# Kernel optimization log

Hardware: AMD Instinct MI355X
Metric: run time of the kernel (lower is better)

Reference implementation:

```python
import jax, jax.numpy as jnp
import numpy as np

NUM_HEADS = 16
D_MODEL = 1024
D_K = D_MODEL // NUM_HEADS
B, S = 2, 2048


def setup_inputs() -> dict:
    key = jax.random.key(0)
    ks = jax.random.split(key, 10)
    q = jax.random.normal(ks[0], (B, S, D_MODEL), dtype=jnp.float32)
    k = jax.random.normal(ks[1], (B, S, D_MODEL), dtype=jnp.float32)
    v = jax.random.normal(ks[2], (B, S, D_MODEL), dtype=jnp.float32)
    # causal mask, 1 = keep, 0 = masked (masked_fill(mask==0, -1e9))
    mask = jnp.tril(jnp.ones((S, S), dtype=jnp.int32))[None, None, :, :]
    # Linear weights ~ N(0, 0.02); biases left at torch default-ish small uniform
    std = 0.02
    Wq = jax.random.normal(ks[3], (D_MODEL, D_MODEL), dtype=jnp.float32) * std
    Wk = jax.random.normal(ks[4], (D_MODEL, D_MODEL), dtype=jnp.float32) * std
    Wv = jax.random.normal(ks[5], (D_MODEL, D_MODEL), dtype=jnp.float32) * std
    bound = 1.0 / np.sqrt(D_MODEL)
    bq = jax.random.uniform(ks[6], (D_MODEL,), jnp.float32, -bound, bound)
    bk = jax.random.uniform(ks[7], (D_MODEL,), jnp.float32, -bound, bound)
    bv = jax.random.uniform(ks[8], (D_MODEL,), jnp.float32, -bound, bound)
    return {"q": q, "k": k, "v": v, "mask": mask,
            "Wq": Wq, "bq": bq, "Wk": Wk, "bk": bk, "Wv": Wv, "bv": bv}


def reference(q, k, v, mask, Wq, bq, Wk, bk, Wv, bv):
    # projections (torch Linear: x @ W.T + b), split heads -> [B, H, S, Dk]
    def proj(x, W, b):
        y = x @ W.T + b
        return y.reshape(B, S, NUM_HEADS, D_K).transpose(0, 2, 1, 3)

    qh, kh, vh = proj(q, Wq, bq), proj(k, Wk, bk), proj(v, Wv, bv)
    scores = jnp.einsum('bhqd,bhkd->bhqk', qh, kh) / jnp.sqrt(jnp.float32(D_K))
    scores = jnp.where(mask == 0, jnp.float32(-1e9), scores)
    p = jax.nn.softmax(scores, axis=-1)
    # dropout is identity in eval mode
    x = jnp.einsum('bhqk,bhkd->bhqd', p, vh)  # [B, H, S, Dk]
    return x.transpose(0, 2, 1, 3).reshape(B, S, D_MODEL)
```

## Files before the change

### kernel.cpp

```cpp
#include <hip/hip_runtime.h>

#define B_ 2
#define H_ 16
#define S_ 2048
#define DM 1024
#define DK 64
#define NX (4096 * 1024)
#define NW (1024 * 1024)

typedef unsigned short u16;
typedef __attribute__((ext_vector_type(8))) short bf16x8;
typedef __attribute__((ext_vector_type(8))) unsigned short u16x8;
typedef __attribute__((ext_vector_type(4))) unsigned short u16x4;
typedef __attribute__((ext_vector_type(2))) unsigned int u32x2;
typedef __attribute__((ext_vector_type(4))) unsigned int u32x4;
typedef __attribute__((ext_vector_type(4))) float f32x4;
typedef __attribute__((ext_vector_type(16))) float f32x16;

__device__ inline u16 f2bf(float f) {
  union { float f; unsigned int u; } c; c.f = f;
  unsigned int u = c.u;
  u += 0x7fffu + ((u >> 16) & 1u);
  return (u16)(u >> 16);
}

__device__ inline u16x8 cvt8(const float* __restrict__ src) {
  const float4 a = *reinterpret_cast<const float4*>(src);
  const float4 b = *reinterpret_cast<const float4*>(src + 4);
  u16x8 r;
  r[0] = f2bf(a.x); r[1] = f2bf(a.y); r[2] = f2bf(a.z); r[3] = f2bf(a.w);
  r[4] = f2bf(b.x); r[5] = f2bf(b.y); r[6] = f2bf(b.z); r[7] = f2bf(b.w);
  return r;
}

__device__ inline void glds16(const u16* g, u16* l) {
  __builtin_amdgcn_global_load_lds(
      (const __attribute__((address_space(1))) unsigned int*)g,
      (__attribute__((address_space(3))) unsigned int*)l, 16, 0, 0);
}

__device__ inline unsigned cvtpk(float lo, float hi) {
  unsigned r;
  asm("v_cvt_pk_bf16_f32 %0, %1, %2" : "=v"(r) : "v"(lo), "v"(hi));
  return r;
}

#if __has_builtin(__builtin_amdgcn_permlane32_swap)
__device__ inline void plswap(unsigned& a, unsigned& b) {
  auto r = __builtin_amdgcn_permlane32_swap(a, b, false, false);
  a = r[0]; b = r[1];
}
#else
__device__ inline void plswap(unsigned& a, unsigned& b) {
  const unsigned pa = (unsigned)__shfl_xor((int)a, 32, 64);
  const unsigned pb = (unsigned)__shfl_xor((int)b, 32, 64);
  const bool hi = (threadIdx.x & 32) != 0;
  const unsigned na = hi ? pb : a;
  const unsigned nb = hi ? b : pa;
  a = na; b = nb;
}
#endif

__global__ __launch_bounds__(256) void cvt_kernel(
    const float* __restrict__ q, const float* __restrict__ k, const float* __restrict__ v,
    const float* __restrict__ Wq, const float* __restrict__ Wk, const float* __restrict__ Wv,
    u16* __restrict__ Xq, u16* __restrict__ Xk, u16* __restrict__ Xv,
    u16* __restrict__ Wqb, u16* __restrict__ Wkb, u16* __restrict__ Wvb)
{
  const int t = blockIdx.y;
  const float* src = (t == 0) ? q : (t == 1) ? k : (t == 2) ? v
                   : (t == 3) ? Wq : (t == 4) ? Wk : Wv;
  u16* dst = (t == 0) ? Xq : (t == 1) ? Xk : (t == 2) ? Xv
           : (t == 3) ? Wqb : (t == 4) ? Wkb : Wvb;
  const int n = (t < 3) ? NX : NW;
  const int idx = (blockIdx.x * 256 + threadIdx.x) * 8;
  if (idx >= n) return;
  *reinterpret_cast<u16x8*>(&dst[idx]) = cvt8(&src[idx]);
}

__global__ __launch_bounds__(256) void proj_kernel(
    const u16* __restrict__ Xq, const u16* __restrict__ Xk, const u16* __restrict__ Xv,
    const u16* __restrict__ Wqb, const u16* __restrict__ Wkb, const u16* __restrict__ Wvb,
    const float* __restrict__ bq, const float* __restrict__ bk, const float* __restrict__ bv,
    u16* __restrict__ Qh, u16* __restrict__ Kh, u16* __restrict__ Vh)
{
  const int z = blockIdx.z;
  const u16* X      = (z == 0) ? Xq : (z == 1) ? Xk : Xv;
  const u16* W      = (z == 0) ? Wqb : (z == 1) ? Wkb : Wvb;
  const float* bias = (z == 0) ? bq : (z == 1) ? bk : bv;
  u16* out          = (z == 0) ? Qh : (z == 1) ? Kh : Vh;
  const float scale = (z == 0) ? 0.18033688f : 1.0f;

  __shared__ __align__(16) u16 Xs[128 * 32];
  __shared__ __align__(16) u16 Ws[128 * 32];

  const int tid = threadIdx.x;
  const int lane = tid & 63;
  const int w = tid >> 6;
  const int wy = w >> 1, wx = w & 1;
  const int m0 = blockIdx.y * 128;
  const int n0 = blockIdx.x * 128;
  const int ml = lane & 15;
  const int qd = lane >> 4;

  f32x4 acc[4][4] = {};

  for (int kb = 0; kb < DM; kb += 32) {
    __syncthreads();
    #pragma unroll
    for (int p = 0; p < 2; ++p) {
      const int c = p * 4 + w;
      const int row = c * 16 + (lane >> 2);
      const int col = kb + (lane & 3) * 8;
      glds16(&X[(size_t)(m0 + row) * DM + col], &Xs[c * 512]);
      glds16(&W[(size_t)(n0 + row) * DM + col], &Ws[c * 512]);
    }
    __syncthreads();
    bf16x8 a[4], bfr[4];
    #pragma unroll
    for (int i = 0; i < 4; ++i)
      a[i] = *reinterpret_cast<const bf16x8*>(&Xs[(wy * 64 + i * 16 + ml) * 32 + qd * 8]);
    #pragma unroll
    for (int j = 0; j < 4; ++j)
      bfr[j] = *reinterpret_cast<const bf16x8*>(&Ws[(wx * 64 + j * 16 + ml) * 32 + qd * 8]);
    #pragma unroll
    for (int i = 0; i < 4; ++i)
      #pragma unroll
      for (int j = 0; j < 4; ++j)
        acc[i][j] = __builtin_amdgcn_mfma_f32_16x16x32_bf16(a[i], bfr[j], acc[i][j], 0, 0, 0);
  }

  #pragma unroll
  for (int j = 0; j < 4; ++j) {
    const int n = n0 + wx * 64 + j * 16 + ml;
    const float badd = bias[n];
    const int h = n >> 6, d = n & 63;
    #pragma unroll
    for (int i = 0; i < 4; ++i) {
      #pragma unroll
      for (int r = 0; r < 4; ++r) {
        const int m = m0 + wy * 64 + i * 16 + qd * 4 + r;
        const int bi = m >> 11, s = m & 2047;
        out[((bi * H_ + h) * S_ + s) * DK + d] = f2bf((acc[i][j][r] + badd) * scale);
      }
    }
  }
}

__global__ __launch_bounds__(256) void transpose_kernel(
    const u16* __restrict__ Vh, u16* __restrict__ Vt)
{
  __shared__ __align__(16) u16 T[64 * 72];
  const int t = threadIdx.x;
  const int st = blockIdx.x, bh = blockIdx.y;
  {
    const int r = t >> 2, c = (t & 3) * 16;
    const u16* src = &Vh[((size_t)bh * S_ + st * 64 + r) * DK + c];
    *reinterpret_cast<u16x8*>(&T[r * 72 + c])     = *reinterpret_cast<const u16x8*>(src);
    *reinterpret_cast<u16x8*>(&T[r * 72 + c + 8]) = *reinterpret_cast<const u16x8*>(src + 8);
  }
  __syncthreads();
  {
    const int d = t >> 2, s0 = (t & 3) * 16;
    u16x8 a, b;
    #pragma unroll
    for (int i = 0; i < 8; ++i) a[i] = T[(s0 + i) * 72 + d];
    #pragma unroll
    for (int i = 0; i < 8; ++i) b[i] = T[(s0 + 8 + i) * 72 + d];
    u16* dst = &Vt[((size_t)bh * DK + d) * S_ + st * 64 + s0];
    *reinterpret_cast<u16x8*>(dst)     = a;
    *reinterpret_cast<u16x8*>(dst + 8) = b;
  }
}

__global__ __launch_bounds__(256) void attn_kernel(
    const u16* __restrict__ Qh, const u16* __restrict__ Kh,
    const u16* __restrict__ Vt, float* __restrict__ out)
{
  __shared__ __align__(16) u16 Ks[2][64 * 64];
  __shared__ __align__(16) u16 Vs[64 * 64];
  __shared__ float Ls[4][32];

  const int tid  = threadIdx.x;
  const int lane = tid & 63;
  const int w    = tid >> 6;
  const int l31  = lane & 31, hi = lane >> 5;
  const int x7   = l31 & 7;

  const int fid = blockIdx.x;
  const int bh  = (fid & 7) * 4 + ((fid >> 3) & 3);
  const int qtl = fid >> 5;
  const int qt  = (qtl < 8) ? (15 - 2 * qtl) : (2 * (qtl - 8));
  const int b   = bh >> 4, h = bh & 15;
  const int R0  = qt * 128;
  const int nt  = 2 * qt + 2;

  bf16x8 qa[4];
  {
    const u16* qp = &Qh[((size_t)bh * S_ + R0 + w * 32 + l31) * DK + hi * 8];
    #pragma unroll
    for (int s = 0; s < 4; ++s)
      qa[s] = *reinterpret_cast<const bf16x8*>(qp + s * 16);
  }
  asm volatile("s_waitcnt vmcnt(0)" ::: "memory");

  const u16* kb0 = Kh + (size_t)bh * S_ * DK;
  const u16* vb0 = Vt + (size_t)bh * DK * S_;
  const int r0 = tid >> 3, r1 = r0 + 32;
  const int cs = (tid & 7) ^ (r0 & 7);
  const u16* sK0 = kb0 + r0 * DK + cs * 8;
  const u16* sK1 = kb0 + r1 * DK + cs * 8;

  const int vu = tid & 7;
  const int vswz = (vu ^ (r0 & 7)) * 8;
  const u16* sV0 = vb0 + (size_t)r0 * S_ + vu * 8;
  const u16* sV1 = vb0 + (size_t)r1 * S_ + vu * 8;
  u16* vd0 = &Vs[r0 * 64 + vswz];
  u16* vd1 = &Vs[r1 * 64 + vswz];

  f32x16 oacc0 = {}, oacc1 = {};
  float lsum = 0.f;

  u16x8 vreg0 = *reinterpret_cast<const u16x8*>(sV0);
  u16x8 vreg1 = *reinterpret_cast<const u16x8*>(sV1);
  glds16(sK0, &Ks[0][tid * 8]);
  glds16(sK1, &Ks[0][2048 + tid * 8]);
  sK0 += 4096; sK1 += 4096; sV0 += 64; sV1 += 64;
  asm volatile("s_waitcnt vmcnt(0)" ::: "memory");

  int cur = 0;
  for (int t = 0; t < nt; ++t) {
    *reinterpret_cast<u16x8*>(vd0) = vreg0;
    *reinterpret_cast<u16x8*>(vd1) = vreg1;
    if (t + 1 < nt) {
      vreg0 = *reinterpret_cast<const u16x8*>(sV0);
      vreg1 = *reinterpret_cast<const u16x8*>(sV1);
      glds16(sK0, &Ks[cur ^ 1][tid * 8]);
      glds16(sK1, &Ks[cur ^ 1][2048 + tid * 8]);
      sK0 += 4096; sK1 += 4096; sV0 += 64; sV1 += 64;
    }
    asm volatile("s_waitcnt lgkmcnt(0)" ::: "memory");
    __builtin_amdgcn_s_barrier();
    asm volatile("" ::: "memory");

    const u16* Kb = Ks[cur];

    const int base  = R0 + w * 32 - t * 64;
    const int ksmax = (base + 31) >> 5;
    const int ksm   = (ksmax > 1) ? 1 : ksmax;

    if (ksm >= 0) {
      f32x16 sfr[2];
      __builtin_amdgcn_s_setprio(1);
      #pragma unroll
      for (int ks = 0; ks < 2; ++ks) {
        if (ks > ksm) break;
        const int rb = (ks * 32 + l31) * 64;
        f32x16 sf = {};
        #pragma unroll
        for (int s = 0; s < 4; ++s) {
          const bf16x8 af = *reinterpret_cast<const bf16x8*>(
              &Kb[rb + ((2 * s + hi) ^ x7) * 8]);
          sf = __builtin_amdgcn_mfma_f32_32x32x16_bf16(af, qa[s], sf, 0, 0, 0);
        }
        sfr[ks] = sf;
      }
      __builtin_amdgcn_s_setprio(0);

      unsigned pku[2][4][2];
      #pragma unroll
      for (int ks = 0; ks < 2; ++ks) {
        if (ks > ksm) break;
        const int Dg = base + l31 - 32 * ks - 4 * hi;
        const bool full = (base >= 32 * ks + 31);
        float e[16];
        #pragma unroll
        for (int r = 0; r < 16; ++r) {
          const int rk = (r & 3) + 8 * (r >> 2);
          const float ex = __builtin_amdgcn_exp2f(sfr[ks][r]);
          e[r] = (full || rk <= Dg) ? ex : 0.f;
        }
        float a01 = 0.f;
        #pragma unroll
        for (int r = 0; r < 16; ++r) a01 += e[r];
        lsum += a01;
        #pragma unroll
        for (int m = 0; m < 4; ++m) {
          pku[ks][m][0] = cvtpk(e[4 * m], e[4 * m + 1]);
          pku[ks][m][1] = cvtpk(e[4 * m + 2], e[4 * m + 3]);
        }
      }

      const int smax = 2 * ksm + 1;
      #pragma unroll
      for (int s = 0; s < 4; ++s) {
        if (s > smax) break;
        const int ks = s >> 1, p = s & 1;
        unsigned w0 = pku[ks][2 * p][0],     w1v = pku[ks][2 * p][1];
        unsigned w2 = pku[ks][2 * p + 1][0], w3  = pku[ks][2 * p + 1][1];
        plswap(w0, w2);
        plswap(w1v, w3);
        u32x4 paw; paw[0] = w0; paw[1] = w1v; paw[2] = w2; paw[3] = w3;
        const bf16x8 pa = *reinterpret_cast<const bf16x8*>(&paw);
        const int uv = ((2 * s + hi) ^ x7) * 8;
        const bf16x8 vb0f = *reinterpret_cast<const bf16x8*>(&Vs[l31 * 64 + uv]);
        const bf16x8 vb1f = *reinterpret_cast<const bf16x8*>(&Vs[(32 + l31) * 64 + uv]);
        __builtin_amdgcn_s_setprio(1);
        oacc0 = __builtin_amdgcn_mfma_f32_32x32x16_bf16(pa, vb0f, oacc0, 0, 0, 0);
        oacc1 = __builtin_amdgcn_mfma_f32_32x32x16_bf16(pa, vb1f, oacc1, 0, 0, 0);
        __builtin_amdgcn_s_setprio(0);
      }
    }

    asm volatile("" ::: "memory");
    __builtin_amdgcn_s_barrier();
    asm volatile("s_waitcnt vmcnt(0)" ::: "memory");
    cur ^= 1;
  }

  const float lt = lsum + __shfl_xor(lsum, 32, 64);
  if (hi == 0) Ls[w][l31] = 1.0f / lt;
  #pragma unroll
  for (int r = 0; r < 16; ++r) {
    const int rq = (r & 3) + 8 * (r >> 2) + 4 * hi;
    const float inv = Ls[w][rq];
    const int srow = R0 + w * 32 + rq;
    float* op = &out[(size_t)(b * S_ + srow) * DM + h * DK + l31];
    op[0]  = oacc0[r] * inv;
    op[32] = oacc1[r] * inv;
  }
}

extern "C" void kernel_launch(void* const* d_in, const int* in_sizes, int n_in,
                              void* d_out, int out_size, void* d_ws, size_t ws_size,
                              hipStream_t stream) {
  const float* q  = (const float*)d_in[0];
  const float* k  = (const float*)d_in[1];
  const float* v  = (const float*)d_in[2];
  const float* Wq = (const float*)d_in[4];
  const float* bq = (const float*)d_in[5];
  const float* Wk = (const float*)d_in[6];
  const float* bk = (const float*)d_in[7];
  const float* Wv = (const float*)d_in[8];
  const float* bv = (const float*)d_in[9];

  u16* Xq  = (u16*)d_ws;
  u16* Xk  = Xq + NX;
  u16* Xv  = Xk + NX;
  u16* Wqb = Xv + NX;
  u16* Wkb = Wqb + NW;
  u16* Wvb = Wkb + NW;
  u16* Qh  = Wvb + NW;
  u16* Kh  = Qh + NX;
  u16* Vh  = Kh + NX;
  u16* Vt  = Xq;

  cvt_kernel<<<dim3(NX / (256 * 8), 6), 256, 0, stream>>>(
      q, k, v, Wq, Wk, Wv, Xq, Xk, Xv, Wqb, Wkb, Wvb);
  proj_kernel<<<dim3(DM / 128, (B_ * S_) / 128, 3), 256, 0, stream>>>(
      Xq, Xk, Xv, Wqb, Wkb, Wvb, bq, bk, bv, Qh, Kh, Vh);
  transpose_kernel<<<dim3(S_ / 64, B_ * H_), 256, 0, stream>>>(Vh, Vt);
  attn_kernel<<<dim3(512), 256, 0, stream>>>(
      Qh, Kh, Vt, (float*)d_out);
}
```

Baseline: 219.3 us.

## Halve attention block to 64 query rows with 2 waves and 1024 blocks

```diff
diff --git a/kernel.cpp b/kernel.cpp
--- a/kernel.cpp
+++ b/kernel.cpp
@@ -12,7 +12,6 @@
 typedef __attribute__((ext_vector_type(8))) short bf16x8;
 typedef __attribute__((ext_vector_type(8))) unsigned short u16x8;
 typedef __attribute__((ext_vector_type(4))) unsigned short u16x4;
-typedef __attribute__((ext_vector_type(2))) unsigned int u32x2;
 typedef __attribute__((ext_vector_type(4))) unsigned int u32x4;
 typedef __attribute__((ext_vector_type(4))) float f32x4;
 typedef __attribute__((ext_vector_type(16))) float f32x16;
@@ -173,13 +172,13 @@
   }
 }
 
-__global__ __launch_bounds__(256) void attn_kernel(
+__global__ __launch_bounds__(128) void attn_kernel(
     const u16* __restrict__ Qh, const u16* __restrict__ Kh,
     const u16* __restrict__ Vt, float* __restrict__ out)
 {
   __shared__ __align__(16) u16 Ks[2][64 * 64];
   __shared__ __align__(16) u16 Vs[64 * 64];
-  __shared__ float Ls[4][32];
+  __shared__ float Ls[2][32];
 
   const int tid  = threadIdx.x;
   const int lane = tid & 63;
@@ -189,11 +188,10 @@
 
   const int fid = blockIdx.x;
   const int bh  = (fid & 7) * 4 + ((fid >> 3) & 3);
-  const int qtl = fid >> 5;
-  const int qt  = (qtl < 8) ? (15 - 2 * qtl) : (2 * (qtl - 8));
+  const int qt  = 31 - (fid >> 5);
   const int b   = bh >> 4, h = bh & 15;
-  const int R0  = qt * 128;
-  const int nt  = 2 * qt + 2;
+  const int R0  = qt * 64;
+  const int nt  = qt + 1;
 
   bf16x8 qa[4];
   {
@@ -206,38 +204,38 @@
 
   const u16* kb0 = Kh + (size_t)bh * S_ * DK;
   const u16* vb0 = Vt + (size_t)bh * DK * S_;
-  const int r0 = tid >> 3, r1 = r0 + 32;
-  const int cs = (tid & 7) ^ (r0 & 7);
-  const u16* sK0 = kb0 + r0 * DK + cs * 8;
-  const u16* sK1 = kb0 + r1 * DK + cs * 8;
-
-  const int vu = tid & 7;
-  const int vswz = (vu ^ (r0 & 7)) * 8;
-  const u16* sV0 = vb0 + (size_t)r0 * S_ + vu * 8;
-  const u16* sV1 = vb0 + (size_t)r1 * S_ + vu * 8;
-  u16* vd0 = &Vs[r0 * 64 + vswz];
-  u16* vd1 = &Vs[r1 * 64 + vswz];
+  const int rb8 = tid >> 3;
+  const int cs  = (tid & 7) ^ (rb8 & 7);
+  const u16* sKp = kb0 + rb8 * DK + cs * 8;
+  const u16* sVp = vb0 + (size_t)rb8 * S_ + (tid & 7) * 8;
+  u16* vdp = &Vs[rb8 * 64 + cs * 8];
 
   f32x16 oacc0 = {}, oacc1 = {};
   float lsum = 0.f;
 
-  u16x8 vreg0 = *reinterpret_cast<const u16x8*>(sV0);
-  u16x8 vreg1 = *reinterpret_cast<const u16x8*>(sV1);
-  glds16(sK0, &Ks[0][tid * 8]);
-  glds16(sK1, &Ks[0][2048 + tid * 8]);
-  sK0 += 4096; sK1 += 4096; sV0 += 64; sV1 += 64;
+  u16x8 vreg[4];
+  #pragma unroll
+  for (int p = 0; p < 4; ++p)
+    vreg[p] = *reinterpret_cast<const u16x8*>(sVp + (size_t)p * 16 * S_);
+  #pragma unroll
+  for (int p = 0; p < 4; ++p)
+    glds16(sKp + p * 1024, &Ks[0][(p * 128 + tid) * 8]);
   asm volatile("s_waitcnt vmcnt(0)" ::: "memory");
 
   int cur = 0;
   for (int t = 0; t < nt; ++t) {
-    *reinterpret_cast<u16x8*>(vd0) = vreg0;
-    *reinterpret_cast<u16x8*>(vd1) = vreg1;
+    #pragma unroll
+    for (int p = 0; p < 4; ++p)
+      *reinterpret_cast<u16x8*>(vdp + p * 1024) = vreg[p];
     if (t + 1 < nt) {
-      vreg0 = *reinterpret_cast<const u16x8*>(sV0);
-      vreg1 = *reinterpret_cast<const u16x8*>(sV1);
-      glds16(sK0, &Ks[cur ^ 1][tid * 8]);
-      glds16(sK1, &Ks[cur ^ 1][2048 + tid * 8]);
-      sK0 += 4096; sK1 += 4096; sV0 += 64; sV1 += 64;
+      #pragma unroll
+      for (int p = 0; p < 4; ++p)
+        vreg[p] = *reinterpret_cast<const u16x8*>(
+            sVp + (size_t)p * 16 * S_ + (t + 1) * 64);
+      #pragma unroll
+      for (int p = 0; p < 4; ++p)
+        glds16(sKp + (size_t)(t + 1) * 4096 + p * 1024,
+               &Ks[cur ^ 1][(p * 128 + tid) * 8]);
     }
     asm volatile("s_waitcnt lgkmcnt(0)" ::: "memory");
     __builtin_amdgcn_s_barrier();
@@ -249,7 +247,7 @@
     const int ksmax = (base + 31) >> 5;
     const int ksm   = (ksmax > 1) ? 1 : ksmax;
 
-    if (ksm >= 0) {
+    {
       f32x16 sfr[2];
       __builtin_amdgcn_s_setprio(1);
       #pragma unroll
@@ -360,6 +358,6 @@
   proj_kernel<<<dim3(DM / 128, (B_ * S_) / 128, 3), 256, 0, stream>>>(
       Xq, Xk, Xv, Wqb, Wkb, Wvb, bq, bk, bv, Qh, Kh, Vh);
   transpose_kernel<<<dim3(S_ / 64, B_ * H_), 256, 0, stream>>>(Vh, Vt);
-  attn_kernel<<<dim3(512), 256, 0, stream>>>(
+  attn_kernel<<<dim3(1024), 128, 0, stream>>>(
       Qh, Kh, Vt, (float*)d_out);
 }
```

Result: no change. 219.0 us (-0.1%).
